# Performance work log

Measured on AMD Instinct MI355X. Metric: run time of the kernel, lower is better.

Reference implementation:

```python
import jax, jax.numpy as jnp
import numpy as np

N_NODES = 100000
N_EDGES = 600000
F_IN, HID, CLS = 128, 128, 16


def sage_conv(x, src, dst, W_l, b_l, W_r, n_nodes):
    # mean aggregation of neighbor features: message x[src] scattered to dst
    msg = x[src]                                              # [E, F]
    agg = jax.ops.segment_sum(msg, dst, num_segments=n_nodes)  # [N, F]
    deg = jax.ops.segment_sum(jnp.ones((src.shape[0],), x.dtype), dst, num_segments=n_nodes)
    agg = agg / jnp.maximum(deg, 1.0)[:, None]
    # PyG SAGEConv: lin_l(agg) (with bias) + lin_r(x_root) (no bias)
    return agg @ W_l + b_l + x @ W_r


def setup_inputs() -> dict:
    key = jax.random.key(0)
    ks = jax.random.split(key, 6)
    x = jax.random.normal(ks[0], (N_NODES, F_IN), jnp.float32)
    edge_index = jax.random.randint(ks[1], (2, N_EDGES), 0, N_NODES, dtype=jnp.int64)
    s1 = 1.0 / np.sqrt(F_IN)
    s2 = 1.0 / np.sqrt(HID)
    return {
        "x": x,
        "edge_index": edge_index,
        "W1_l": jax.random.normal(ks[2], (F_IN, HID), jnp.float32) * s1,
        "b1": jnp.zeros((HID,), jnp.float32),
        "W1_r": jax.random.normal(ks[3], (F_IN, HID), jnp.float32) * s1,
        "W2_l": jax.random.normal(ks[4], (HID, CLS), jnp.float32) * s2,
        "b2": jnp.zeros((CLS,), jnp.float32),
        "W2_r": jax.random.normal(ks[5], (HID, CLS), jnp.float32) * s2,
    }


def reference(x, edge_index, W1_l, b1, W1_r, W2_l, b2, W2_r):
    n = x.shape[0]
    src, dst = edge_index[0], edge_index[1]
    h = sage_conv(x, src, dst, W1_l, b1, W1_r, n)
    h = jax.nn.relu(h)
    # F.dropout(training=self.training): identity in eval mode
    out = sage_conv(h, src, dst, W2_l, b2, W2_r, n)
    return jax.nn.log_softmax(out, axis=1)
```

## Files before the change

### kernel.cpp

```cpp
#include <hip/hip_runtime.h>
#include <cstdint>

#define N_NODES 100000
#define N_PAD 100096
#define N_EDGES 600000
#define F 128
#define CLS 16
#define CAP 64

typedef short bf16x8 __attribute__((ext_vector_type(8)));
typedef float f32x4 __attribute__((ext_vector_type(4)));
typedef float f32x2 __attribute__((ext_vector_type(2)));

__device__ inline float bf2f(unsigned int lo16) { return __uint_as_float(lo16 << 16); }
__device__ inline unsigned short f2b(float f) {
    unsigned int u = __float_as_uint(f);
    return (unsigned short)((u + 0x7fffu + ((u >> 16) & 1u)) >> 16);
}

__global__ __launch_bounds__(256) void init_k(int* __restrict__ deg,
                                              const float* __restrict__ x,
                                              unsigned short* __restrict__ xb,
                                              unsigned int* __restrict__ xf8,
                                              const float* __restrict__ W1l,
                                              const float* __restrict__ W1r,
                                              const float* __restrict__ W2l,
                                              const float* __restrict__ W2r,
                                              unsigned short* __restrict__ w1t,
                                              unsigned short* __restrict__ w2t) {
    int b = blockIdx.x;
    if (b < 98) {
        int i = b * 1024 + threadIdx.x * 4;
#pragma unroll
        for (int k = 0; k < 4; k++)
            if (i + k < N_NODES) deg[i + k] = 0;
    } else if (b < 12598) {
        int i = (b - 98) * 256 + threadIdx.x;
        if (i < N_NODES * F / 4) {
            float4 v = ((const float4*)x)[i];
            ushort4 o;
            o.x = f2b(v.x); o.y = f2b(v.y); o.z = f2b(v.z); o.w = f2b(v.w);
            ((ushort4*)xb)[i] = o;
            int p8 = __builtin_amdgcn_cvt_pk_fp8_f32(v.x, v.y, 0, false);
            p8 = __builtin_amdgcn_cvt_pk_fp8_f32(v.z, v.w, p8, true);
            xf8[i] = (unsigned int)p8;
        }
    } else if (b < 12726) {
        int idx = (b - 12598) * 256 + threadIdx.x;
        int n = idx >> 8, k = idx & 255;
        float v = (k < F) ? W1l[k * F + n] : W1r[(k - F) * F + n];
        int ct = n >> 4, m = n & 15;
        int half = k >> 7, ks = (k >> 5) & 3, quad = (k >> 3) & 3, j = k & 7;
        w1t[(ct * 8 + ks * 2 + half) * 512 + (quad * 16 + m) * 8 + j] = f2b(v);
    } else {
        int idx = (b - 12726) * 256 + threadIdx.x;
        if (idx < 32 * F) {
            int n = idx >> 7, k = idx & 127;
            float v = (n < CLS) ? W2l[k * CLS + n] : W2r[k * CLS + (n - CLS)];
            int tile = n >> 4, m = n & 15;
            int ks = (k >> 5) & 3, quad = (k >> 3) & 3, j = k & 7;
            w2t[(tile * 4 + ks) * 512 + (quad * 16 + m) * 8 + j] = f2b(v);
        }
    }
}

__global__ void fill_k(const int* __restrict__ src, const int* __restrict__ dst,
                       int* __restrict__ deg, int* __restrict__ bucket) {
    int e = blockIdx.x * blockDim.x + threadIdx.x;
    if (e < N_EDGES) {
        int d = dst[e];
        int slot = atomicAdd(&deg[d], 1);
        if (slot < CAP) bucket[d * CAP + slot] = src[e];
    }
}

__global__ __launch_bounds__(256) void agg_b_k(const unsigned char* __restrict__ feat8,
                                               const int* __restrict__ deg,
                                               const int* __restrict__ bucket,
                                               unsigned short* __restrict__ outagg) {
    int node = blockIdx.x * 4 + (threadIdx.x >> 6);
    int lane = threadIdx.x & 63;
    int r = lane >> 4;
    int f8 = (lane & 15) * 8;
    const int* bk = bucket + node * CAP;

    int d_raw = deg[node];
    int nb0 = min(max(bk[r], 0), N_NODES - 1);
    int nb1 = min(max(bk[4 + r], 0), N_NODES - 1);
    uint2 v0 = *(const uint2*)(feat8 + (size_t)nb0 * F + f8);
    uint2 v1 = *(const uint2*)(feat8 + (size_t)nb1 * F + f8);

    int d = min(d_raw, CAP);
    float acc[8] = {0.f, 0.f, 0.f, 0.f, 0.f, 0.f, 0.f, 0.f};
#define ACC8(vv) { f32x2 p; \
    p = __builtin_amdgcn_cvt_pk_f32_fp8((int)(vv).x, false); acc[0] += p.x; acc[1] += p.y; \
    p = __builtin_amdgcn_cvt_pk_f32_fp8((int)(vv).x, true);  acc[2] += p.x; acc[3] += p.y; \
    p = __builtin_amdgcn_cvt_pk_f32_fp8((int)(vv).y, false); acc[4] += p.x; acc[5] += p.y; \
    p = __builtin_amdgcn_cvt_pk_f32_fp8((int)(vv).y, true);  acc[6] += p.x; acc[7] += p.y; }
    if (r < d) ACC8(v0);
    if (4 + r < d) ACC8(v1);
    for (int j = 8; j < d; j += 8) {
        int i0 = j + r, i1 = j + 4 + r;
        bool ok0 = i0 < d, ok1 = i1 < d;
        int m0 = bk[ok0 ? i0 : 0];
        int m1 = bk[ok1 ? i1 : 0];
        uint2 w0 = *(const uint2*)(feat8 + (size_t)m0 * F + f8);
        uint2 w1 = *(const uint2*)(feat8 + (size_t)m1 * F + f8);
        if (ok0) ACC8(w0);
        if (ok1) ACC8(w1);
    }
#undef ACC8
#pragma unroll
    for (int i = 0; i < 8; i++) {
        acc[i] += __shfl_xor(acc[i], 16);
        acc[i] += __shfl_xor(acc[i], 32);
    }
    if (r == 0) {
        float inv = 1.0f / fmaxf((float)d, 1.0f);
        uint4 o;
        o.x = (unsigned int)f2b(acc[0] * inv) | ((unsigned int)f2b(acc[1] * inv) << 16);
        o.y = (unsigned int)f2b(acc[2] * inv) | ((unsigned int)f2b(acc[3] * inv) << 16);
        o.z = (unsigned int)f2b(acc[4] * inv) | ((unsigned int)f2b(acc[5] * inv) << 16);
        o.w = (unsigned int)f2b(acc[6] * inv) | ((unsigned int)f2b(acc[7] * inv) << 16);
        *(uint4*)(outagg + (size_t)node * F + f8) = o;
    }
}

__global__ __launch_bounds__(256) void gemm_fused(const unsigned short* __restrict__ Ab,
                                                  const unsigned short* __restrict__ Xb,
                                                  const unsigned short* __restrict__ Wt,
                                                  const float* __restrict__ bias,
                                                  const unsigned short* __restrict__ Wt2,
                                                  unsigned short* __restrict__ trLb,
                                                  float* __restrict__ trR) {
    __shared__ unsigned short sh[128 * 132];
    int tid = threadIdx.x;
    int wave = tid >> 6, lane = tid & 63;
    int row0 = blockIdx.x * 128 + wave * 32;
    int m = lane & 15, quad = lane >> 4;
    int koff = quad * 8;

    const unsigned short* pa0 = Ab + (size_t)(row0 + m) * F + koff;
    const unsigned short* pa1 = pa0 + 16 * F;
    const unsigned short* px0 = Xb + (size_t)(row0 + m) * F + koff;
    const unsigned short* px1 = px0 + 16 * F;
    const unsigned short* pw = Wt + lane * 8;

    f32x4 acc0[8], acc1[8];
#pragma unroll
    for (int ct = 0; ct < 8; ct++) { acc0[ct] = (f32x4){0,0,0,0}; acc1[ct] = (f32x4){0,0,0,0}; }

#pragma unroll
    for (int ks = 0; ks < 4; ks++) {
        bf16x8 a0 = *(const bf16x8*)(const void*)(pa0 + ks * 32);
        bf16x8 a1 = *(const bf16x8*)(const void*)(pa1 + ks * 32);
        bf16x8 x0 = *(const bf16x8*)(const void*)(px0 + ks * 32);
        bf16x8 x1 = *(const bf16x8*)(const void*)(px1 + ks * 32);
#pragma unroll
        for (int ct = 0; ct < 8; ct++) {
            bf16x8 bl = *(const bf16x8*)(const void*)(pw + (ct * 8 + ks * 2 + 0) * 512);
            bf16x8 br = *(const bf16x8*)(const void*)(pw + (ct * 8 + ks * 2 + 1) * 512);
            acc0[ct] = __builtin_amdgcn_mfma_f32_16x16x32_bf16(a0, bl, acc0[ct], 0, 0, 0);
            acc1[ct] = __builtin_amdgcn_mfma_f32_16x16x32_bf16(a1, bl, acc1[ct], 0, 0, 0);
            acc0[ct] = __builtin_amdgcn_mfma_f32_16x16x32_bf16(x0, br, acc0[ct], 0, 0, 0);
            acc1[ct] = __builtin_amdgcn_mfma_f32_16x16x32_bf16(x1, br, acc1[ct], 0, 0, 0);
        }
    }

    int lr0 = wave * 32 + quad * 4;
#pragma unroll
    for (int ct = 0; ct < 8; ct++) {
        int n = ct * 16 + m;
        float bv = bias[n];
#pragma unroll
        for (int r = 0; r < 4; r++) {
            sh[(lr0 + r) * 132 + n]      = f2b(fmaxf(acc0[ct][r] + bv, 0.f));
            sh[(lr0 + 16 + r) * 132 + n] = f2b(fmaxf(acc1[ct][r] + bv, 0.f));
        }
    }
    __syncthreads();

    const unsigned short* hl0 = sh + (wave * 32 + m) * 132 + koff;
    const unsigned short* hl1 = sh + (wave * 32 + 16 + m) * 132 + koff;
    const unsigned short* pw2 = Wt2 + lane * 8;

    f32x4 al0 = (f32x4){0,0,0,0}, al1 = (f32x4){0,0,0,0};
    f32x4 ar0 = (f32x4){0,0,0,0}, ar1 = (f32x4){0,0,0,0};
#pragma unroll
    for (int ks = 0; ks < 4; ks++) {
        bf16x8 h0 = *(const bf16x8*)(const void*)(hl0 + ks * 32);
        bf16x8 h1 = *(const bf16x8*)(const void*)(hl1 + ks * 32);
        bf16x8 wl = *(const bf16x8*)(const void*)(pw2 + (0 * 4 + ks) * 512);
        bf16x8 wr = *(const bf16x8*)(const void*)(pw2 + (1 * 4 + ks) * 512);
        al0 = __builtin_amdgcn_mfma_f32_16x16x32_bf16(h0, wl, al0, 0, 0, 0);
        al1 = __builtin_amdgcn_mfma_f32_16x16x32_bf16(h1, wl, al1, 0, 0, 0);
        ar0 = __builtin_amdgcn_mfma_f32_16x16x32_bf16(h0, wr, ar0, 0, 0, 0);
        ar1 = __builtin_amdgcn_mfma_f32_16x16x32_bf16(h1, wr, ar1, 0, 0, 0);
    }
    int r0 = row0 + quad * 4;
#pragma unroll
    for (int r = 0; r < 4; r++) {
        trLb[(size_t)(r0 + r) * CLS + m]      = f2b(al0[r]);
        trLb[(size_t)(r0 + 16 + r) * CLS + m] = f2b(al1[r]);
        trR[(size_t)(r0 + r) * CLS + m]       = ar0[r];
        trR[(size_t)(r0 + 16 + r) * CLS + m]  = ar1[r];
    }
}

__global__ __launch_bounds__(256) void agg2sm_k(const unsigned short* __restrict__ trLb,
                                                const float* __restrict__ trR,
                                                const int* __restrict__ deg,
                                                const int* __restrict__ bucket,
                                                const float* __restrict__ b2,
                                                float* __restrict__ out) {
    int node = blockIdx.x * 4 + (threadIdx.x >> 6);
    int lane = threadIdx.x & 63;
    int r = lane >> 2;
    int cq = (lane & 3) * 4;
    const int* bk = bucket + node * CAP;

    int d_raw = deg[node];
    int nb = min(max(bk[r], 0), N_NODES - 1);
    uint2 v = *(const uint2*)(trLb + (size_t)nb * CLS + cq);
    float4 selfR = *(const float4*)(trR + (size_t)node * CLS + cq);

    int d = min(d_raw, CAP);
    float4 acc = {0.f, 0.f, 0.f, 0.f};
    if (r < d) {
        acc.x += bf2f(v.x & 0xffffu); acc.y += bf2f(v.x >> 16);
        acc.z += bf2f(v.y & 0xffffu); acc.w += bf2f(v.y >> 16);
    }
    for (int j = 16; j < d; j += 16) {
        int idx = j + r;
        bool valid = idx < d;
        int m2 = bk[valid ? idx : 0];
        uint2 w = *(const uint2*)(trLb + (size_t)m2 * CLS + cq);
        if (valid) {
            acc.x += bf2f(w.x & 0xffffu); acc.y += bf2f(w.x >> 16);
            acc.z += bf2f(w.y & 0xffffu); acc.w += bf2f(w.y >> 16);
        }
    }
#pragma unroll
    for (int off = 4; off <= 32; off <<= 1) {
        acc.x += __shfl_xor(acc.x, off);
        acc.y += __shfl_xor(acc.y, off);
        acc.z += __shfl_xor(acc.z, off);
        acc.w += __shfl_xor(acc.w, off);
    }
    float inv = 1.0f / fmaxf((float)d, 1.0f);
    float4 bb = *(const float4*)(b2 + cq);
    float vx = acc.x * inv + selfR.x + bb.x;
    float vy = acc.y * inv + selfR.y + bb.y;
    float vz = acc.z * inv + selfR.z + bb.z;
    float vw = acc.w * inv + selfR.w + bb.w;
    float mx = fmaxf(fmaxf(vx, vy), fmaxf(vz, vw));
    mx = fmaxf(mx, __shfl_xor(mx, 1));
    mx = fmaxf(mx, __shfl_xor(mx, 2));
    float sm = __expf(vx - mx) + __expf(vy - mx) + __expf(vz - mx) + __expf(vw - mx);
    sm += __shfl_xor(sm, 1);
    sm += __shfl_xor(sm, 2);
    float lg = __logf(sm);
    if (r == 0) {
        float4 o = {vx - mx - lg, vy - mx - lg, vz - mx - lg, vw - mx - lg};
        *(float4*)(out + (size_t)node * CLS + cq) = o;
    }
}


extern "C" void kernel_launch(void* const* d_in, const int* in_sizes, int n_in,
                              void* d_out, int out_size, void* d_ws, size_t ws_size,
                              hipStream_t stream) {
    const float* x   = (const float*)d_in[0];
    const int*   ei  = (const int*)d_in[1];
    const float* W1l = (const float*)d_in[2];
    const float* b1  = (const float*)d_in[3];
    const float* W1r = (const float*)d_in[4];
    const float* W2l = (const float*)d_in[5];
    const float* b2  = (const float*)d_in[6];
    const float* W2r = (const float*)d_in[7];
    float* out = (float*)d_out;

    const int* src = ei;
    const int* dst = ei + N_EDGES;

    char* ws = (char*)d_ws;
    size_t off = 0;
    auto alloc = [&](size_t bytes) { char* p = ws + off; off += (bytes + 127) / 128 * 128; return p; };
    int* deg    = (int*)alloc((size_t)N_NODES * 4);
    int* bucket = (int*)alloc((size_t)N_NODES * CAP * 4);
    unsigned short* xb   = (unsigned short*)alloc((size_t)N_PAD * F * 2);
    unsigned char*  xf8  = (unsigned char*)alloc((size_t)N_PAD * F);
    unsigned short* aggb = (unsigned short*)alloc((size_t)N_PAD * F * 2);
    unsigned short* trLb = (unsigned short*)alloc((size_t)N_PAD * CLS * 2);
    float*          trR  = (float*)alloc((size_t)N_PAD * CLS * 4);
    unsigned short* w1t  = (unsigned short*)alloc((size_t)F * 256 * 2);
    unsigned short* w2t  = (unsigned short*)alloc((size_t)32 * F * 2);

    init_k<<<12743, 256, 0, stream>>>(deg, x, xb, (unsigned int*)xf8,
                                      W1l, W1r, W2l, W2r, w1t, w2t);
    fill_k<<<(N_EDGES + 255) / 256, 256, 0, stream>>>(src, dst, deg, bucket);
    agg_b_k<<<N_NODES / 4, 256, 0, stream>>>(xf8, deg, bucket, aggb);
    gemm_fused<<<N_PAD / 128, 256, 0, stream>>>(aggb, xb, w1t, b1, w2t, trLb, trR);
    agg2sm_k<<<N_NODES / 4, 256, 0, stream>>>(trLb, trR, deg, bucket, b2, out);
}
```

Measured before the change: 227.7 us.

## Aggregate layer-1 neighbors from bf16 features with 16 lanes per node

Drops the fp8 copy of x and has the first aggregation gather from the existing bf16 copy, removing the fp8 conversion and its writes from init. The aggregation kernel now gives each node 16 lanes instead of 64, and each lane walks all neighbors in chunks of 8 with vectorized bucket index loads, so no cross-lane shuffle reduction is needed. Each gather now reads twice the bytes per neighbor, and a node's neighbors are processed serially within its lanes, which puts more pressure on memory latency.

Result: faster. 221.9 us (-2.6%).

```diff
diff --git a/kernel.cpp b/kernel.cpp
--- a/kernel.cpp
+++ b/kernel.cpp
@@ -10,7 +10,6 @@
 
 typedef short bf16x8 __attribute__((ext_vector_type(8)));
 typedef float f32x4 __attribute__((ext_vector_type(4)));
-typedef float f32x2 __attribute__((ext_vector_type(2)));
 
 __device__ inline float bf2f(unsigned int lo16) { return __uint_as_float(lo16 << 16); }
 __device__ inline unsigned short f2b(float f) {
@@ -21,7 +20,6 @@
 __global__ __launch_bounds__(256) void init_k(int* __restrict__ deg,
                                               const float* __restrict__ x,
                                               unsigned short* __restrict__ xb,
-                                              unsigned int* __restrict__ xf8,
                                               const float* __restrict__ W1l,
                                               const float* __restrict__ W1r,
                                               const float* __restrict__ W2l,
@@ -41,9 +39,6 @@
             ushort4 o;
             o.x = f2b(v.x); o.y = f2b(v.y); o.z = f2b(v.z); o.w = f2b(v.w);
             ((ushort4*)xb)[i] = o;
-            int p8 = __builtin_amdgcn_cvt_pk_fp8_f32(v.x, v.y, 0, false);
-            p8 = __builtin_amdgcn_cvt_pk_fp8_f32(v.z, v.w, p8, true);
-            xf8[i] = (unsigned int)p8;
         }
     } else if (b < 12726) {
         int idx = (b - 12598) * 256 + threadIdx.x;
@@ -74,56 +69,61 @@
     }
 }
 
-__global__ __launch_bounds__(256) void agg_b_k(const unsigned char* __restrict__ feat8,
+__global__ __launch_bounds__(256) void agg_b_k(const unsigned short* __restrict__ feat,
                                                const int* __restrict__ deg,
                                                const int* __restrict__ bucket,
                                                unsigned short* __restrict__ outagg) {
-    int node = blockIdx.x * 4 + (threadIdx.x >> 6);
-    int lane = threadIdx.x & 63;
-    int r = lane >> 4;
-    int f8 = (lane & 15) * 8;
+    int tid = threadIdx.x;
+    int node = blockIdx.x * 16 + (tid >> 4);
+    int f8 = (tid & 15) * 8;
     const int* bk = bucket + node * CAP;
 
     int d_raw = deg[node];
-    int nb0 = min(max(bk[r], 0), N_NODES - 1);
-    int nb1 = min(max(bk[4 + r], 0), N_NODES - 1);
-    uint2 v0 = *(const uint2*)(feat8 + (size_t)nb0 * F + f8);
-    uint2 v1 = *(const uint2*)(feat8 + (size_t)nb1 * F + f8);
-
+    float acc[8] = {0.f, 0.f, 0.f, 0.f, 0.f, 0.f, 0.f, 0.f};
     int d = min(d_raw, CAP);
-    float acc[8] = {0.f, 0.f, 0.f, 0.f, 0.f, 0.f, 0.f, 0.f};
-#define ACC8(vv) { f32x2 p; \
-    p = __builtin_amdgcn_cvt_pk_f32_fp8((int)(vv).x, false); acc[0] += p.x; acc[1] += p.y; \
-    p = __builtin_amdgcn_cvt_pk_f32_fp8((int)(vv).x, true);  acc[2] += p.x; acc[3] += p.y; \
-    p = __builtin_amdgcn_cvt_pk_f32_fp8((int)(vv).y, false); acc[4] += p.x; acc[5] += p.y; \
-    p = __builtin_amdgcn_cvt_pk_f32_fp8((int)(vv).y, true);  acc[6] += p.x; acc[7] += p.y; }
-    if (r < d) ACC8(v0);
-    if (4 + r < d) ACC8(v1);
-    for (int j = 8; j < d; j += 8) {
-        int i0 = j + r, i1 = j + 4 + r;
-        bool ok0 = i0 < d, ok1 = i1 < d;
-        int m0 = bk[ok0 ? i0 : 0];
-        int m1 = bk[ok1 ? i1 : 0];
-        uint2 w0 = *(const uint2*)(feat8 + (size_t)m0 * F + f8);
-        uint2 w1 = *(const uint2*)(feat8 + (size_t)m1 * F + f8);
-        if (ok0) ACC8(w0);
-        if (ok1) ACC8(w1);
-    }
+
+    for (int j0 = 0; j0 < d; j0 += 8) {
+        int4 b0 = *(const int4*)(bk + j0);
+        int4 b1 = *(const int4*)(bk + j0 + 4);
+        int n0 = min(max(b0.x, 0), N_NODES - 1);
+        int n1 = min(max(b0.y, 0), N_NODES - 1);
+        int n2 = min(max(b0.z, 0), N_NODES - 1);
+        int n3 = min(max(b0.w, 0), N_NODES - 1);
+        int n4 = min(max(b1.x, 0), N_NODES - 1);
+        int n5 = min(max(b1.y, 0), N_NODES - 1);
+        int n6 = min(max(b1.z, 0), N_NODES - 1);
+        int n7 = min(max(b1.w, 0), N_NODES - 1);
+        uint4 v0 = *(const uint4*)(feat + (size_t)n0 * F + f8);
+        uint4 v1 = *(const uint4*)(feat + (size_t)n1 * F + f8);
+        uint4 v2 = *(const uint4*)(feat + (size_t)n2 * F + f8);
+        uint4 v3 = *(const uint4*)(feat + (size_t)n3 * F + f8);
+        uint4 v4 = *(const uint4*)(feat + (size_t)n4 * F + f8);
+        uint4 v5 = *(const uint4*)(feat + (size_t)n5 * F + f8);
+        uint4 v6 = *(const uint4*)(feat + (size_t)n6 * F + f8);
+        uint4 v7 = *(const uint4*)(feat + (size_t)n7 * F + f8);
+#define ACC8(vv) { \
+    acc[0] += bf2f((vv).x & 0xffffu); acc[1] += bf2f((vv).x >> 16); \
+    acc[2] += bf2f((vv).y & 0xffffu); acc[3] += bf2f((vv).y >> 16); \
+    acc[4] += bf2f((vv).z & 0xffffu); acc[5] += bf2f((vv).z >> 16); \
+    acc[6] += bf2f((vv).w & 0xffffu); acc[7] += bf2f((vv).w >> 16); }
+        int rem = d - j0;
+        if (rem > 0) ACC8(v0);
+        if (rem > 1) ACC8(v1);
+        if (rem > 2) ACC8(v2);
+        if (rem > 3) ACC8(v3);
+        if (rem > 4) ACC8(v4);
+        if (rem > 5) ACC8(v5);
+        if (rem > 6) ACC8(v6);
+        if (rem > 7) ACC8(v7);
 #undef ACC8
-#pragma unroll
-    for (int i = 0; i < 8; i++) {
-        acc[i] += __shfl_xor(acc[i], 16);
-        acc[i] += __shfl_xor(acc[i], 32);
-    }
-    if (r == 0) {
-        float inv = 1.0f / fmaxf((float)d, 1.0f);
-        uint4 o;
-        o.x = (unsigned int)f2b(acc[0] * inv) | ((unsigned int)f2b(acc[1] * inv) << 16);
-        o.y = (unsigned int)f2b(acc[2] * inv) | ((unsigned int)f2b(acc[3] * inv) << 16);
-        o.z = (unsigned int)f2b(acc[4] * inv) | ((unsigned int)f2b(acc[5] * inv) << 16);
-        o.w = (unsigned int)f2b(acc[6] * inv) | ((unsigned int)f2b(acc[7] * inv) << 16);
-        *(uint4*)(outagg + (size_t)node * F + f8) = o;
-    }
+    }
+    float inv = 1.0f / fmaxf((float)d, 1.0f);
+    uint4 o;
+    o.x = (unsigned int)f2b(acc[0] * inv) | ((unsigned int)f2b(acc[1] * inv) << 16);
+    o.y = (unsigned int)f2b(acc[2] * inv) | ((unsigned int)f2b(acc[3] * inv) << 16);
+    o.z = (unsigned int)f2b(acc[4] * inv) | ((unsigned int)f2b(acc[5] * inv) << 16);
+    o.w = (unsigned int)f2b(acc[6] * inv) | ((unsigned int)f2b(acc[7] * inv) << 16);
+    *(uint4*)(outagg + (size_t)node * F + f8) = o;
 }
 
 __global__ __launch_bounds__(256) void gemm_fused(const unsigned short* __restrict__ Ab,
@@ -289,17 +289,15 @@
     int* deg    = (int*)alloc((size_t)N_NODES * 4);
     int* bucket = (int*)alloc((size_t)N_NODES * CAP * 4);
     unsigned short* xb   = (unsigned short*)alloc((size_t)N_PAD * F * 2);
-    unsigned char*  xf8  = (unsigned char*)alloc((size_t)N_PAD * F);
     unsigned short* aggb = (unsigned short*)alloc((size_t)N_PAD * F * 2);
     unsigned short* trLb = (unsigned short*)alloc((size_t)N_PAD * CLS * 2);
     float*          trR  = (float*)alloc((size_t)N_PAD * CLS * 4);
     unsigned short* w1t  = (unsigned short*)alloc((size_t)F * 256 * 2);
     unsigned short* w2t  = (unsigned short*)alloc((size_t)32 * F * 2);
 
-    init_k<<<12743, 256, 0, stream>>>(deg, x, xb, (unsigned int*)xf8,
-                                      W1l, W1r, W2l, W2r, w1t, w2t);
+    init_k<<<12743, 256, 0, stream>>>(deg, x, xb, W1l, W1r, W2l, W2r, w1t, w2t);
     fill_k<<<(N_EDGES + 255) / 256, 256, 0, stream>>>(src, dst, deg, bucket);
-    agg_b_k<<<N_NODES / 4, 256, 0, stream>>>(xf8, deg, bucket, aggb);
+    agg_b_k<<<N_NODES / 16, 256, 0, stream>>>(xb, deg, bucket, aggb);
     gemm_fused<<<N_PAD / 128, 256, 0, stream>>>(aggb, xb, w1t, b1, w2t, trLb, trR);
     agg2sm_k<<<N_NODES / 4, 256, 0, stream>>>(trLb, trR, deg, bucket, b2, out);
 }
```
